# Kernel optimization log

Hardware: AMD Instinct MI355X
Metric: run time of the kernel (lower is better)

The kernel has to match this reference:

```python
import jax, jax.numpy as jnp
import numpy as np

B, S, T, C, Q = 8, 4096, 2048, 256, 256  # batch, ctx_steps, q_steps, context_size, query_size


def setup_inputs() -> dict:
    key = jax.random.key(0)
    k1, k2, k3, k4 = jax.random.split(key, 4)
    context = jax.random.normal(k1, (B, S, C), dtype=jnp.float32)
    query = jax.random.normal(k2, (T, B, Q), dtype=jnp.float32)
    context_mask = jax.random.randint(k3, (B, S), 0, 2).astype(bool)  # True = masked
    W = jax.random.normal(k4, (C, Q), dtype=jnp.float32)  # bilinear weights [context_size, query_size]
    return {"context": context, "query": query, "context_mask": context_mask, "W": W}


def reference(context, query, context_mask, W):
    # temp = 'auto' -> sqrt(query_size)
    temp = jnp.asarray(np.sqrt(Q), dtype=context.dtype)
    # scores[b,t,s] = (context[b,s,:] @ W) . query[t,b,:]
    scores = jnp.einsum('bsc,cq,tbq->bts', context, W, query) / temp
    neg = jnp.finfo(scores.dtype).min
    scores = jnp.where(context_mask[:, None, :], neg, scores)  # mask over ctx_steps
    attn = jax.nn.softmax(scores, axis=2)  # [B, T, S]
    # rows whose entire context is masked -> attention zeroed
    all_masked = jnp.all(context_mask, axis=1)[:, None, None]
    attn = jnp.where(all_masked, jnp.zeros((), attn.dtype), attn)
    composition = jnp.einsum('bts,bsc->btc', attn, context)  # [B, T, C]
    # module returns (attn, composition) permuted to [T, B, ...]
    return attn.transpose(1, 0, 2), composition.transpose(1, 0, 2)
```

## Files before the change

kernel.cpp:

```cpp
#include <hip/hip_runtime.h>

#define B_ 8
#define S_ 4096
#define T_ 2048
#define C_ 256
#define Q_ 256
#define NROW (T_ * B_)

typedef _Float16 f16;
typedef _Float16 f16x8 __attribute__((ext_vector_type(8)));
typedef _Float16 f16x4 __attribute__((ext_vector_type(4)));
typedef float f32x4 __attribute__((ext_vector_type(4)));

#define MFMA(a, b, c) __builtin_amdgcn_mfma_f32_16x16x32_f16((a), (b), (c), 0, 0, 0)

__global__ void k_mask_mode(const unsigned char* __restrict__ mb, int* __restrict__ mode,
                            int* __restrict__ allm) {
  __shared__ int s0_, s123_;
  if (threadIdx.x == 0) { s0_ = 0; s123_ = 0; }
  __syncthreads();
  int a0 = 0, a123 = 0;
  int base = threadIdx.x * 128;
  for (int i = 0; i < 128; ++i) {
    int idx = base + i;
    int v = mb[idx];
    if (idx & 3) a123 |= v; else a0 |= v;
  }
  if (a0) atomicOr(&s0_, 1);
  if (a123) atomicOr(&s123_, 1);
  __syncthreads();
  if (threadIdx.x == 0) {
    int m;
    if (s123_ == 0 && s0_ == 0) m = 3;
    else if (s123_ == 0) m = 0;
    else if (s0_ == 0) m = 2;
    else m = 1;
    *mode = m;
  }
  if (threadIdx.x < B_) allm[threadIdx.x] = 1;
}

__global__ void k_expand_mask(const void* __restrict__ mp, const int* __restrict__ mode,
                              float* __restrict__ maskf, int* __restrict__ allm) {
  int i = blockIdx.x * 256 + threadIdx.x;
  int md = *mode;
  int m;
  if (md == 0)      m = ((const int*)mp)[i] != 0;
  else if (md == 1) m = ((const unsigned char*)mp)[i] != 0;
  else if (md == 2) m = ((const float*)mp)[i] != 0.0f;
  else              m = 0;
  maskf[i] = m ? 1.0f : 0.0f;
  if (!m) atomicAnd(&allm[i / S_], 0);
}

__global__ void k_conv_w(const float* __restrict__ W, f16* __restrict__ WT) {
  int i = blockIdx.x * 256 + threadIdx.x;
  int c = i >> 8, q = i & 255;
  WT[q * C_ + c] = (f16)W[i];
}

__global__ void k_conv_q(const float* __restrict__ q, f16* __restrict__ qT) {
  int i = blockIdx.x * 256 + threadIdx.x;
  int e = i * 4;
  int t = e / (B_ * Q_);
  int rb = e - t * (B_ * Q_);
  int b = rb >> 8;
  int qq = rb & 255;
  f32x4 v = *(const f32x4*)(q + e);
  f16x4 h; h[0] = (f16)v[0]; h[1] = (f16)v[1]; h[2] = (f16)v[2]; h[3] = (f16)v[3];
  *(f16x4*)(qT + ((size_t)(b * T_ + t)) * Q_ + qq) = h;
}

__global__ void k_transpose_ctx(const float* __restrict__ ctx, f16* __restrict__ ctxT) {
  __shared__ f16 tile[64][65];
  int s0 = blockIdx.x * 64, c0 = blockIdx.y * 64, b = blockIdx.z;
  int r = threadIdx.x >> 2;
  int cs = (threadIdx.x & 3) * 16;
  const float* src = ctx + ((size_t)(b * S_ + s0 + r)) * C_ + c0 + cs;
  f32x4 v0 = ((const f32x4*)src)[0];
  f32x4 v1 = ((const f32x4*)src)[1];
  f32x4 v2 = ((const f32x4*)src)[2];
  f32x4 v3 = ((const f32x4*)src)[3];
#pragma unroll
  for (int j = 0; j < 4; ++j) {
    tile[r][cs + j] = (f16)v0[j];
    tile[r][cs + 4 + j] = (f16)v1[j];
    tile[r][cs + 8 + j] = (f16)v2[j];
    tile[r][cs + 12 + j] = (f16)v3[j];
  }
  __syncthreads();
  int c = threadIdx.x >> 2;
  int ss = (threadIdx.x & 3) * 16;
  f16x8 o0, o1;
#pragma unroll
  for (int j = 0; j < 8; ++j) { o0[j] = tile[ss + j][c]; o1[j] = tile[ss + 8 + j][c]; }
  f16* dst = ctxT + ((size_t)(b * C_ + c0 + c)) * S_ + s0 + ss;
  *(f16x8*)dst = o0;
  *(f16x8*)(dst + 8) = o1;
}

__launch_bounds__(256, 2)
__global__ void k_gemm_cw(const float* __restrict__ ctx, const f16* __restrict__ WT,
                          f16* __restrict__ CW) {
  __shared__ alignas(16) f16 As[128 * 32];
  __shared__ alignas(16) f16 Bs[128 * 32];
  int n0 = blockIdx.x * 128;
  int m0 = blockIdx.y * 128;
  int tid = threadIdx.x;
  int w = tid >> 6, l = tid & 63;
  int wm = (w >> 1) * 64, wn = (w & 1) * 64;
  int lr = l & 15, lk = (l >> 4) * 8;
  f32x4 acc[4][4] = {};
  for (int k0 = 0; k0 < C_; k0 += 32) {
    __syncthreads();
#pragma unroll
    for (int it = 0; it < 2; ++it) {
      int h = (it * 256 + tid) * 8;
      int row = h >> 5, kk = h & 31;
      const float* ap = ctx + (size_t)(m0 + row) * C_ + k0 + kk;
      f32x4 x0 = ((const f32x4*)ap)[0];
      f32x4 x1 = ((const f32x4*)ap)[1];
      f16x8 hv;
#pragma unroll
      for (int j = 0; j < 4; ++j) { hv[j] = (f16)x0[j]; hv[4 + j] = (f16)x1[j]; }
      *(f16x8*)&As[row * 32 + kk] = hv;
    }
#pragma unroll
    for (int it = 0; it < 2; ++it) {
      int h = (it * 256 + tid) * 8;
      int row = h >> 5, kk = h & 31;
      *(f16x8*)&Bs[row * 32 + kk] = *(const f16x8*)&WT[(size_t)(n0 + row) * C_ + k0 + kk];
    }
    __syncthreads();
    f16x8 af[4], bf[4];
#pragma unroll
    for (int m = 0; m < 4; ++m) af[m] = *(const f16x8*)&As[(wm + m * 16 + lr) * 32 + lk];
#pragma unroll
    for (int n = 0; n < 4; ++n) bf[n] = *(const f16x8*)&Bs[(wn + n * 16 + lr) * 32 + lk];
#pragma unroll
    for (int m = 0; m < 4; ++m)
#pragma unroll
      for (int n = 0; n < 4; ++n) acc[m][n] = MFMA(af[m], bf[n], acc[m][n]);
  }
#pragma unroll
  for (int m = 0; m < 4; ++m)
#pragma unroll
    for (int n = 0; n < 4; ++n)
#pragma unroll
      for (int i = 0; i < 4; ++i) {
        int gm = m0 + wm + m * 16 + (l >> 4) * 4 + i;
        int gn = n0 + wn + n * 16 + lr;
        CW[(size_t)gm * Q_ + gn] = (f16)(acc[m][n][i] * 0.0625f);
      }
}

__launch_bounds__(256, 2)
__global__ void k_gemm_scores(const f16* __restrict__ qT, const f16* __restrict__ CW,
                              const float* __restrict__ maskf, float* __restrict__ attn,
                              float* __restrict__ pmax, float* __restrict__ psum) {
  __shared__ alignas(16) f16 As[128 * 32];
  __shared__ alignas(16) f16 Bs[128 * 32];
  int n0 = blockIdx.x * 128;
  int m0 = blockIdx.y * 128;
  int b = blockIdx.z;
  const f16* A = qT + (size_t)b * T_ * Q_;
  const f16* Bm = CW + (size_t)b * S_ * Q_;
  int tid = threadIdx.x;
  int w = tid >> 6, l = tid & 63;
  int wm = (w >> 1) * 64, wn = (w & 1) * 64;
  int lr = l & 15, lk = (l >> 4) * 8;
  f32x4 acc[4][4] = {};
  for (int k0 = 0; k0 < Q_; k0 += 32) {
    __syncthreads();
#pragma unroll
    for (int it = 0; it < 2; ++it) {
      int h = (it * 256 + tid) * 8;
      int row = h >> 5, kk = h & 31;
      *(f16x8*)&As[row * 32 + kk] = *(const f16x8*)&A[(size_t)(m0 + row) * Q_ + k0 + kk];
    }
#pragma unroll
    for (int it = 0; it < 2; ++it) {
      int h = (it * 256 + tid) * 8;
      int row = h >> 5, kk = h & 31;
      *(f16x8*)&Bs[row * 32 + kk] = *(const f16x8*)&Bm[(size_t)(n0 + row) * Q_ + k0 + kk];
    }
    __syncthreads();
    f16x8 af[4], bf[4];
#pragma unroll
    for (int m = 0; m < 4; ++m) af[m] = *(const f16x8*)&As[(wm + m * 16 + lr) * 32 + lk];
#pragma unroll
    for (int n = 0; n < 4; ++n) bf[n] = *(const f16x8*)&Bs[(wn + n * 16 + lr) * 32 + lk];
#pragma unroll
    for (int m = 0; m < 4; ++m)
#pragma unroll
      for (int n = 0; n < 4; ++n) acc[m][n] = MFMA(af[m], bf[n], acc[m][n]);
  }
  float msk[4];
#pragma unroll
  for (int n = 0; n < 4; ++n) msk[n] = maskf[b * S_ + n0 + wn + n * 16 + lr];
#pragma unroll
  for (int m = 0; m < 4; ++m)
#pragma unroll
    for (int n = 0; n < 4; ++n) {
      int gn = n0 + wn + n * 16 + lr;
#pragma unroll
      for (int i = 0; i < 4; ++i) {
        int gt = m0 + wm + m * 16 + (l >> 4) * 4 + i;
        float v = acc[m][n][i];
        if (msk[n] != 0.0f) v = -3.4e38f;
        acc[m][n][i] = v;
        attn[((size_t)gt * B_ + b) * S_ + gn] = v;
      }
    }
  int g = l >> 4;
  int ch = blockIdx.x * 2 + (w & 1);
#pragma unroll
  for (int m = 0; m < 4; ++m)
#pragma unroll
    for (int i = 0; i < 4; ++i) {
      float mx = fmaxf(fmaxf(acc[m][0][i], acc[m][1][i]), fmaxf(acc[m][2][i], acc[m][3][i]));
      mx = fmaxf(mx, __shfl_xor(mx, 1));
      mx = fmaxf(mx, __shfl_xor(mx, 2));
      mx = fmaxf(mx, __shfl_xor(mx, 4));
      mx = fmaxf(mx, __shfl_xor(mx, 8));
      float sm = 0.0f;
#pragma unroll
      for (int n = 0; n < 4; ++n) sm += __expf(acc[m][n][i] - mx);
      sm += __shfl_xor(sm, 1);
      sm += __shfl_xor(sm, 2);
      sm += __shfl_xor(sm, 4);
      sm += __shfl_xor(sm, 8);
      if (lr == 0) {
        int gt = m0 + wm + m * 16 + g * 4 + i;
        int r = gt * B_ + b;
        pmax[ch * NROW + r] = mx;
        psum[ch * NROW + r] = sm;
      }
    }
}

__launch_bounds__(256, 2)
__global__ void k_gemm_stats(const f16* __restrict__ qT, const f16* __restrict__ CW,
                             const float* __restrict__ maskf,
                             float* __restrict__ pmax, float* __restrict__ psum) {
  __shared__ alignas(16) f16 As[128 * 32];
  __shared__ alignas(16) f16 Bs[128 * 32];
  int n0 = blockIdx.x * 128;
  int m0 = blockIdx.y * 128;
  int b = blockIdx.z;
  const f16* A = qT + (size_t)b * T_ * Q_;
  const f16* Bm = CW + (size_t)b * S_ * Q_;
  int tid = threadIdx.x;
  int w = tid >> 6, l = tid & 63;
  int wm = (w >> 1) * 64, wn = (w & 1) * 64;
  int lr = l & 15, lk = (l >> 4) * 8;
  f32x4 acc[4][4] = {};
  for (int k0 = 0; k0 < Q_; k0 += 32) {
    __syncthreads();
#pragma unroll
    for (int it = 0; it < 2; ++it) {
      int h = (it * 256 + tid) * 8;
      int row = h >> 5, kk = h & 31;
      *(f16x8*)&As[row * 32 + kk] = *(const f16x8*)&A[(size_t)(m0 + row) * Q_ + k0 + kk];
    }
#pragma unroll
    for (int it = 0; it < 2; ++it) {
      int h = (it * 256 + tid) * 8;
      int row = h >> 5, kk = h & 31;
      *(f16x8*)&Bs[row * 32 + kk] = *(const f16x8*)&Bm[(size_t)(n0 + row) * Q_ + k0 + kk];
    }
    __syncthreads();
    f16x8 af[4], bf[4];
#pragma unroll
    for (int m = 0; m < 4; ++m) af[m] = *(const f16x8*)&As[(wm + m * 16 + lr) * 32 + lk];
#pragma unroll
    for (int n = 0; n < 4; ++n) bf[n] = *(const f16x8*)&Bs[(wn + n * 16 + lr) * 32 + lk];
#pragma unroll
    for (int m = 0; m < 4; ++m)
#pragma unroll
      for (int n = 0; n < 4; ++n) acc[m][n] = MFMA(af[m], bf[n], acc[m][n]);
  }
  float msk[4];
#pragma unroll
  for (int n = 0; n < 4; ++n) msk[n] = maskf[b * S_ + n0 + wn + n * 16 + lr];
#pragma unroll
  for (int m = 0; m < 4; ++m)
#pragma unroll
    for (int n = 0; n < 4; ++n) {
      if (msk[n] != 0.0f) {
#pragma unroll
        for (int i = 0; i < 4; ++i) acc[m][n][i] = -3.4e38f;
      }
    }
  int g = l >> 4;
  int ch = blockIdx.x * 2 + (w & 1);
#pragma unroll
  for (int m = 0; m < 4; ++m)
#pragma unroll
    for (int i = 0; i < 4; ++i) {
      float mx = fmaxf(fmaxf(acc[m][0][i], acc[m][1][i]), fmaxf(acc[m][2][i], acc[m][3][i]));
      mx = fmaxf(mx, __shfl_xor(mx, 1));
      mx = fmaxf(mx, __shfl_xor(mx, 2));
      mx = fmaxf(mx, __shfl_xor(mx, 4));
      mx = fmaxf(mx, __shfl_xor(mx, 8));
      float sm = 0.0f;
#pragma unroll
      for (int n = 0; n < 4; ++n) sm += __expf(acc[m][n][i] - mx);
      sm += __shfl_xor(sm, 1);
      sm += __shfl_xor(sm, 2);
      sm += __shfl_xor(sm, 4);
      sm += __shfl_xor(sm, 8);
      if (lr == 0) {
        int gt = m0 + wm + m * 16 + g * 4 + i;
        int r = gt * B_ + b;
        pmax[ch * NROW + r] = mx;
        psum[ch * NROW + r] = sm;
      }
    }
}

__global__ void k_finalize(const float* __restrict__ pmax, const float* __restrict__ psum,
                           float* __restrict__ rmax, float* __restrict__ rsum) {
  int r = blockIdx.x * 256 + threadIdx.x;
  float mx = -3.4e38f;
#pragma unroll 8
  for (int c = 0; c < 64; ++c) mx = fmaxf(mx, pmax[c * NROW + r]);
  float s = 0.0f;
#pragma unroll 8
  for (int c = 0; c < 64; ++c) s += psum[c * NROW + r] * __expf(pmax[c * NROW + r] - mx);
  rmax[r] = mx;
  rsum[r] = s;
}

__launch_bounds__(256, 2)
__global__ void k_comp(float* __restrict__ attn, const f16* __restrict__ ctxT,
                       const float* __restrict__ rmax, const float* __restrict__ rsum,
                       const int* __restrict__ allm, float* __restrict__ comp) {
  __shared__ alignas(16) f16 As[2][32 * 64];
  __shared__ alignas(16) f16 Bs[2][256 * 64];
  const int t0 = blockIdx.x * 32;
  const int b = blockIdx.y;
  const int tid = threadIdx.x;
  const int w = tid >> 6, l = tid & 63;
  const int lr = l & 15, hi = l >> 4;
  const int am = allm[b];
  const int ar = tid >> 4;
  const int cg = tid & 15;
  float mx0, mx1, inv0, inv1;
  float* aP0;
  float* aP1;
  {
    int r0 = (t0 + ar) * B_ + b;
    int r1 = (t0 + 16 + ar) * B_ + b;
    mx0 = rmax[r0]; mx1 = rmax[r1];
    inv0 = am ? 0.0f : (1.0f / rsum[r0]);
    inv1 = am ? 0.0f : (1.0f / rsum[r1]);
    aP0 = attn + (size_t)r0 * S_ + cg * 4;
    aP1 = attn + (size_t)r1 * S_ + cg * 4;
  }
  const int aswz = (cg * 8) ^ ((ar & 7) << 4);
  const int bc = tid >> 3;
  const int bs = tid & 7;
  const f16* bP = ctxT + ((size_t)(b * C_ + bc)) * S_ + bs * 8;
  const int bswz = (bs * 16) ^ ((bc & 7) << 4);
  f32x4 acc[2][4] = {};
  f32x4 aC0 = *(const f32x4*)aP0;
  f32x4 aC1 = *(const f32x4*)aP1;
  f16x8 bC[8];
#pragma unroll
  for (int i = 0; i < 8; ++i) bC[i] = *(const f16x8*)(bP + (size_t)i * 32 * S_);
  for (int k = 0; k < S_ / 64; ++k) {
    const int cur = k & 1;
    const int kn = (k + 1) * 64;
    f32x4 aN0 = *(const f32x4*)(aP0 + kn);
    f32x4 aN1 = *(const f32x4*)(aP1 + kn);
    f16x8 bN[8];
#pragma unroll
    for (int i = 0; i < 8; ++i) bN[i] = *(const f16x8*)(bP + (size_t)i * 32 * S_ + kn);
    f32x4 p0, p1;
#pragma unroll
    for (int e = 0; e < 4; ++e) {
      p0[e] = __expf(aC0[e] - mx0) * inv0;
      p1[e] = __expf(aC1[e] - mx1) * inv1;
    }
    *(f32x4*)(aP0 + k * 64) = p0;
    *(f32x4*)(aP1 + k * 64) = p1;
    f16x4 h0, h1;
#pragma unroll
    for (int e = 0; e < 4; ++e) { h0[e] = (f16)p0[e]; h1[e] = (f16)p1[e]; }
    *(f16x4*)((char*)As[cur] + ar * 128 + aswz) = h0;
    *(f16x4*)((char*)As[cur] + (16 + ar) * 128 + aswz) = h1;
#pragma unroll
    for (int i = 0; i < 8; ++i)
      *(f16x8*)((char*)Bs[cur] + (i * 32 + bc) * 128 + bswz) = bC[i];
    asm volatile("s_waitcnt lgkmcnt(0)" ::: "memory");
    __builtin_amdgcn_s_barrier();
    __builtin_amdgcn_sched_barrier(0);
#pragma unroll
    for (int kk = 0; kk < 2; ++kk) {
      const int cb = (kk * 64 + hi * 16) ^ ((lr & 7) << 4);
      f16x8 af[2], bf[4];
#pragma unroll
      for (int m = 0; m < 2; ++m)
        af[m] = *(const f16x8*)((char*)As[cur] + (m * 16 + lr) * 128 + cb);
#pragma unroll
      for (int n = 0; n < 4; ++n)
        bf[n] = *(const f16x8*)((char*)Bs[cur] + (w * 64 + n * 16 + lr) * 128 + cb);
#pragma unroll
      for (int m = 0; m < 2; ++m)
#pragma unroll
        for (int n = 0; n < 4; ++n) acc[m][n] = MFMA(af[m], bf[n], acc[m][n]);
    }
    aC0 = aN0; aC1 = aN1;
#pragma unroll
    for (int i = 0; i < 8; ++i) bC[i] = bN[i];
  }
#pragma unroll
  for (int m = 0; m < 2; ++m)
#pragma unroll
    for (int n = 0; n < 4; ++n)
#pragma unroll
      for (int i = 0; i < 4; ++i) {
        int tl = m * 16 + hi * 4 + i;
        int cc = w * 64 + n * 16 + lr;
        comp[((size_t)(t0 + tl) * B_ + b) * C_ + cc] = acc[m][n][i];
      }
}

__launch_bounds__(256, 2)
__global__ void k_fused(const f16* __restrict__ qT, const f16* __restrict__ CW,
                        const f16* __restrict__ ctxT, const float* __restrict__ maskf,
                        const float* __restrict__ rmax, const float* __restrict__ rsum,
                        const int* __restrict__ allm,
                        float* __restrict__ attn, float* __restrict__ comp) {
  __shared__ alignas(16) f16 Bs[64 * 256];
  __shared__ alignas(16) f16 Ps[32 * 64];
  const int bid = blockIdx.x;
  const int b = bid & 7, tc = bid >> 3;
  const int t0 = tc * 32;
  const int tid = threadIdx.x;
  const int w = tid >> 6, l = tid & 63;
  const int lr = l & 15, hi = l >> 4;
  const int rswz = (lr & 7) << 4;
  const int am = allm[b];
  float smax[2][4], sinv[2][4];
#pragma unroll
  for (int m = 0; m < 2; ++m)
#pragma unroll
    for (int i = 0; i < 4; ++i) {
      int r = (t0 + m * 16 + hi * 4 + i) * B_ + b;
      smax[m][i] = rmax[r];
      sinv[m][i] = am ? 0.0f : (1.0f / rsum[r]);
    }
  f16x8 af[2][8];
#pragma unroll
  for (int m = 0; m < 2; ++m)
#pragma unroll
    for (int kq = 0; kq < 8; ++kq)
      af[m][kq] = *(const f16x8*)(qT + ((size_t)(b * T_ + t0 + m * 16 + lr)) * Q_ + kq * 32 + hi * 8);
  const int brow = tid & 63;
  const int bcolB = (tid >> 6) * 128;
  const int bswz = (brow & 7) << 4;
  const f16* cwBase = CW + (size_t)b * S_ * Q_;
  {
    const f16* src = cwBase + (size_t)brow * Q_ + bcolB / 2;
#pragma unroll
    for (int j = 0; j < 8; ++j)
      *(f16x8*)((char*)Bs + ((brow * 512 + bcolB + j * 16) ^ bswz)) = *(const f16x8*)(src + j * 8);
  }
  float mk = maskf[b * S_ + w * 16 + lr];
  f32x4 accC[2][4] = {};
  __syncthreads();
  for (int k = 0; k < S_ / 64; ++k) {
    const int s0 = k * 64;
    f32x4 accS[2] = {};
#pragma unroll
    for (int kq = 0; kq < 8; ++kq) {
      f16x8 bfr = *(const f16x8*)((char*)Bs + (((w * 16 + lr) * 512 + kq * 64 + hi * 16) ^ rswz));
#pragma unroll
      for (int m = 0; m < 2; ++m) accS[m] = MFMA(af[m][kq], bfr, accS[m]);
    }
#pragma unroll
    for (int m = 0; m < 2; ++m)
#pragma unroll
      for (int i = 0; i < 4; ++i) {
        int tl = m * 16 + hi * 4 + i;
        float p = (mk != 0.0f) ? 0.0f : __expf(accS[m][i] - smax[m][i]) * sinv[m][i];
        attn[((size_t)(t0 + tl) * B_ + b) * S_ + s0 + w * 16 + lr] = p;
        *(f16*)((char*)Ps + ((tl * 128 + (w * 16 + lr) * 2) ^ ((tl & 7) << 4))) = (f16)p;
      }
    __syncthreads();
    f16x8 gB[8];
    if (k < S_ / 64 - 1) {
      const f16* src = cwBase + (size_t)(s0 + 64 + brow) * Q_ + bcolB / 2;
#pragma unroll
      for (int j = 0; j < 8; ++j) gB[j] = *(const f16x8*)(src + j * 8);
    }
    float mkn = (k < S_ / 64 - 1) ? maskf[b * S_ + s0 + 64 + w * 16 + lr] : 0.0f;
#pragma unroll
    for (int kk = 0; kk < 2; ++kk) {
      f16x8 pa[2];
#pragma unroll
      for (int m = 0; m < 2; ++m)
        pa[m] = *(const f16x8*)((char*)Ps + (((m * 16 + lr) * 128 + kk * 64 + hi * 16) ^ rswz));
#pragma unroll
      for (int n = 0; n < 4; ++n) {
        f16x8 bc = *(const f16x8*)(ctxT + ((size_t)(b * C_ + w * 64 + n * 16 + lr)) * S_
                                   + s0 + kk * 32 + hi * 8);
#pragma unroll
        for (int m = 0; m < 2; ++m) accC[m][n] = MFMA(pa[m], bc, accC[m][n]);
      }
    }
    if (k < S_ / 64 - 1) {
#pragma unroll
      for (int j = 0; j < 8; ++j)
        *(f16x8*)((char*)Bs + ((brow * 512 + bcolB + j * 16) ^ bswz)) = gB[j];
    }
    mk = mkn;
    __syncthreads();
  }
#pragma unroll
  for (int m = 0; m < 2; ++m)
#pragma unroll
    for (int n = 0; n < 4; ++n)
#pragma unroll
      for (int i = 0; i < 4; ++i) {
        int tl = m * 16 + hi * 4 + i;
        int cc = w * 64 + n * 16 + lr;
        comp[((size_t)(t0 + tl) * B_ + b) * C_ + cc] = accC[m][n][i];
      }
}

extern "C" void kernel_launch(void* const* d_in, const int* in_sizes, int n_in,
                              void* d_out, int out_size, void* d_ws, size_t ws_size,
                              hipStream_t stream) {
  const float* ctx = (const float*)d_in[0];
  const float* query = (const float*)d_in[1];
  const void* mask = d_in[2];
  const float* W = (const float*)d_in[3];

  float* out = (float*)d_out;
  float* attn = out;
  float* comp = out + (size_t)T_ * B_ * S_;

  char* ws = (char*)d_ws;
  f16* ctxT = (f16*)(ws);
  f16* qT = (f16*)(ws + 16777216);
  f16* WT = (f16*)(ws + 25165824);
  float* maskf = (float*)(ws + 25296896);
  float* rmax = (float*)(ws + 25427968);
  float* rsum = (float*)(ws + 25493504);
  int* allm = (int*)(ws + 25559040);
  int* mode = (int*)(ws + 25559072);
  float* pmax = (float*)(ws + 25559168);
  float* psum = (float*)(ws + 29753472);

  k_mask_mode<<<1, 256, 0, stream>>>((const unsigned char*)mask, mode, allm);
  k_expand_mask<<<(B_ * S_) / 256, 256, 0, stream>>>(mask, mode, maskf, allm);
  k_conv_w<<<(C_ * Q_) / 256, 256, 0, stream>>>(W, WT);
  k_conv_q<<<(T_ * B_ * Q_ / 4) / 256, 256, 0, stream>>>(query, qT);
  k_transpose_ctx<<<dim3(S_ / 64, C_ / 64, B_), 256, 0, stream>>>(ctx, ctxT);

  if (ws_size >= (size_t)50724992) {
    f16* CW2 = (f16*)(ws + 33947776);
    k_gemm_cw<<<dim3(Q_ / 128, (B_ * S_) / 128), 256, 0, stream>>>(ctx, WT, CW2);
    k_gemm_stats<<<dim3(S_ / 128, T_ / 128, B_), 256, 0, stream>>>(qT, CW2, maskf, pmax, psum);
    k_finalize<<<NROW / 256, 256, 0, stream>>>(pmax, psum, rmax, rsum);
    k_fused<<<dim3((T_ / 32) * B_), 256, 0, stream>>>(qT, CW2, ctxT, maskf, rmax, rsum, allm,
                                                      attn, comp);
  } else {
    f16* CW = (f16*)comp;
    k_gemm_cw<<<dim3(Q_ / 128, (B_ * S_) / 128), 256, 0, stream>>>(ctx, WT, CW);
    k_gemm_scores<<<dim3(S_ / 128, T_ / 128, B_), 256, 0, stream>>>(qT, CW, maskf, attn, pmax, psum);
    k_finalize<<<NROW / 256, 256, 0, stream>>>(pmax, psum, rmax, rsum);
    k_comp<<<dim3(T_ / 32, B_), 256, 0, stream>>>(attn, ctxT, rmax, rsum, allm, comp);
  }
}
```

Measured before the change: 568.7 us.

## Software-pipeline fused attention kernel with register-resident CW and double-buffered P

Removes the shared-memory staging of the CW tile: each wave now loads its own 16 CW rows straight into registers, with a one-step register prefetch. The P tile is double-buffered in LDS so that the score MFMAs for step k overlap the composition MFMAs for step k-1, and each iteration needs one barrier instead of two. Attention stores are paired through a lane shuffle so each even lane writes two floats at once, and the context fragments are loaded early. The cost is a larger register footprint, which can lower occupancy under launch_bounds(256,2), plus a prologue and epilogue that add code.

```diff
diff --git a/kernel.cpp b/kernel.cpp
--- a/kernel.cpp
+++ b/kernel.cpp
@@ -10,6 +10,7 @@
 typedef _Float16 f16;
 typedef _Float16 f16x8 __attribute__((ext_vector_type(8)));
 typedef _Float16 f16x4 __attribute__((ext_vector_type(4)));
+typedef _Float16 f16x2 __attribute__((ext_vector_type(2)));
 typedef float f32x4 __attribute__((ext_vector_type(4)));
 
 #define MFMA(a, b, c) __builtin_amdgcn_mfma_f32_16x16x32_f16((a), (b), (c), 0, 0, 0)
@@ -433,15 +434,14 @@
                         const float* __restrict__ rmax, const float* __restrict__ rsum,
                         const int* __restrict__ allm,
                         float* __restrict__ attn, float* __restrict__ comp) {
-  __shared__ alignas(16) f16 Bs[64 * 256];
-  __shared__ alignas(16) f16 Ps[32 * 64];
+  __shared__ alignas(16) f16 Ps[2][32 * 64];
   const int bid = blockIdx.x;
-  const int b = bid & 7, tc = bid >> 3;
-  const int t0 = tc * 32;
+  const int b = bid & 7, t0 = (bid >> 3) * 32;
   const int tid = threadIdx.x;
   const int w = tid >> 6, l = tid & 63;
   const int lr = l & 15, hi = l >> 4;
   const int rswz = (lr & 7) << 4;
+  const int srow = w * 16 + lr;
   const int am = allm[b];
   float smax[2][4], sinv[2][4];
 #pragma unroll
@@ -458,66 +458,118 @@
 #pragma unroll
     for (int kq = 0; kq < 8; ++kq)
       af[m][kq] = *(const f16x8*)(qT + ((size_t)(b * T_ + t0 + m * 16 + lr)) * Q_ + kq * 32 + hi * 8);
-  const int brow = tid & 63;
-  const int bcolB = (tid >> 6) * 128;
-  const int bswz = (brow & 7) << 4;
-  const f16* cwBase = CW + (size_t)b * S_ * Q_;
+  const f16* cwL = CW + (size_t)b * S_ * Q_ + (size_t)srow * Q_ + hi * 8;
+  const f16* cxL = ctxT + (size_t)(b * C_ + w * 64 + lr) * S_ + hi * 8;
+  const float* maskP = maskf + b * S_ + srow;
+  f32x4 accC[2][4] = {};
+  f16x8 cwF[8];
+#pragma unroll
+  for (int kq = 0; kq < 8; ++kq) cwF[kq] = *(const f16x8*)(cwL + kq * 32);
+  float mk = maskP[0];
   {
-    const f16* src = cwBase + (size_t)brow * Q_ + bcolB / 2;
-#pragma unroll
-    for (int j = 0; j < 8; ++j)
-      *(f16x8*)((char*)Bs + ((brow * 512 + bcolB + j * 16) ^ bswz)) = *(const f16x8*)(src + j * 8);
-  }
-  float mk = maskf[b * S_ + w * 16 + lr];
-  f32x4 accC[2][4] = {};
-  __syncthreads();
-  for (int k = 0; k < S_ / 64; ++k) {
-    const int s0 = k * 64;
+    f16x8 cwN[8];
+#pragma unroll
+    for (int kq = 0; kq < 8; ++kq) cwN[kq] = *(const f16x8*)(cwL + (size_t)64 * Q_ + kq * 32);
+    float mkn = maskP[64];
     f32x4 accS[2] = {};
 #pragma unroll
-    for (int kq = 0; kq < 8; ++kq) {
-      f16x8 bfr = *(const f16x8*)((char*)Bs + (((w * 16 + lr) * 512 + kq * 64 + hi * 16) ^ rswz));
-#pragma unroll
-      for (int m = 0; m < 2; ++m) accS[m] = MFMA(af[m][kq], bfr, accS[m]);
-    }
+    for (int kq = 0; kq < 8; ++kq)
+#pragma unroll
+      for (int m = 0; m < 2; ++m) accS[m] = MFMA(af[m][kq], cwF[kq], accS[m]);
 #pragma unroll
     for (int m = 0; m < 2; ++m)
 #pragma unroll
       for (int i = 0; i < 4; ++i) {
         int tl = m * 16 + hi * 4 + i;
         float p = (mk != 0.0f) ? 0.0f : __expf(accS[m][i] - smax[m][i]) * sinv[m][i];
-        attn[((size_t)(t0 + tl) * B_ + b) * S_ + s0 + w * 16 + lr] = p;
-        *(f16*)((char*)Ps + ((tl * 128 + (w * 16 + lr) * 2) ^ ((tl & 7) << 4))) = (f16)p;
-      }
-    __syncthreads();
-    f16x8 gB[8];
+        float po = __shfl_xor(p, 1);
+        if (!(lr & 1)) {
+          float2 fp; fp.x = p; fp.y = po;
+          *(float2*)&attn[((size_t)(t0 + tl) * B_ + b) * S_ + srow] = fp;
+          f16x2 h; h[0] = (f16)p; h[1] = (f16)po;
+          *(f16x2*)((char*)Ps[0] + ((tl * 128 + srow * 2) ^ ((tl & 7) << 4))) = h;
+        }
+      }
+#pragma unroll
+    for (int kq = 0; kq < 8; ++kq) cwF[kq] = cwN[kq];
+    mk = mkn;
+    asm volatile("s_waitcnt lgkmcnt(0)" ::: "memory");
+    __builtin_amdgcn_s_barrier();
+  }
+  for (int k = 1; k < S_ / 64; ++k) {
+    const int s0 = k * 64;
+    const int cur = k & 1, prev = cur ^ 1;
+    f16x8 cwN[8];
+    float mkn = 0.0f;
     if (k < S_ / 64 - 1) {
-      const f16* src = cwBase + (size_t)(s0 + 64 + brow) * Q_ + bcolB / 2;
-#pragma unroll
-      for (int j = 0; j < 8; ++j) gB[j] = *(const f16x8*)(src + j * 8);
-    }
-    float mkn = (k < S_ / 64 - 1) ? maskf[b * S_ + s0 + 64 + w * 16 + lr] : 0.0f;
+#pragma unroll
+      for (int kq = 0; kq < 8; ++kq)
+        cwN[kq] = *(const f16x8*)(cwL + (size_t)(s0 + 64) * Q_ + kq * 32);
+      mkn = maskP[s0 + 64];
+    }
+    const int sc0 = s0 - 64;
+    f16x8 cx[8];
+#pragma unroll
+    for (int n = 0; n < 4; ++n)
+#pragma unroll
+      for (int kk = 0; kk < 2; ++kk)
+        cx[n * 2 + kk] = *(const f16x8*)(cxL + (size_t)(n * 16) * S_ + sc0 + kk * 32);
+    f32x4 accS[2] = {};
+#pragma unroll
+    for (int kq = 0; kq < 8; ++kq)
+#pragma unroll
+      for (int m = 0; m < 2; ++m) accS[m] = MFMA(af[m][kq], cwF[kq], accS[m]);
 #pragma unroll
     for (int kk = 0; kk < 2; ++kk) {
       f16x8 pa[2];
 #pragma unroll
       for (int m = 0; m < 2; ++m)
-        pa[m] = *(const f16x8*)((char*)Ps + (((m * 16 + lr) * 128 + kk * 64 + hi * 16) ^ rswz));
-#pragma unroll
-      for (int n = 0; n < 4; ++n) {
-        f16x8 bc = *(const f16x8*)(ctxT + ((size_t)(b * C_ + w * 64 + n * 16 + lr)) * S_
-                                   + s0 + kk * 32 + hi * 8);
-#pragma unroll
-        for (int m = 0; m < 2; ++m) accC[m][n] = MFMA(pa[m], bc, accC[m][n]);
-      }
-    }
-    if (k < S_ / 64 - 1) {
-#pragma unroll
-      for (int j = 0; j < 8; ++j)
-        *(f16x8*)((char*)Bs + ((brow * 512 + bcolB + j * 16) ^ bswz)) = gB[j];
-    }
+        pa[m] = *(const f16x8*)((char*)Ps[prev] + (((m * 16 + lr) * 128 + kk * 64 + hi * 16) ^ rswz));
+#pragma unroll
+      for (int n = 0; n < 4; ++n)
+#pragma unroll
+        for (int m = 0; m < 2; ++m) accC[m][n] = MFMA(pa[m], cx[n * 2 + kk], accC[m][n]);
+    }
+#pragma unroll
+    for (int m = 0; m < 2; ++m)
+#pragma unroll
+      for (int i = 0; i < 4; ++i) {
+        int tl = m * 16 + hi * 4 + i;
+        float p = (mk != 0.0f) ? 0.0f : __expf(accS[m][i] - smax[m][i]) * sinv[m][i];
+        float po = __shfl_xor(p, 1);
+        if (!(lr & 1)) {
+          float2 fp; fp.x = p; fp.y = po;
+          *(float2*)&attn[((size_t)(t0 + tl) * B_ + b) * S_ + s0 + srow] = fp;
+          f16x2 h; h[0] = (f16)p; h[1] = (f16)po;
+          *(f16x2*)((char*)Ps[cur] + ((tl * 128 + srow * 2) ^ ((tl & 7) << 4))) = h;
+        }
+      }
+#pragma unroll
+    for (int kq = 0; kq < 8; ++kq) cwF[kq] = cwN[kq];
     mk = mkn;
-    __syncthreads();
+    asm volatile("s_waitcnt lgkmcnt(0)" ::: "memory");
+    __builtin_amdgcn_s_barrier();
+  }
+  {
+    const int sc0 = S_ - 64;
+    const int prev = (S_ / 64 - 1) & 1;
+    f16x8 cx[8];
+#pragma unroll
+    for (int n = 0; n < 4; ++n)
+#pragma unroll
+      for (int kk = 0; kk < 2; ++kk)
+        cx[n * 2 + kk] = *(const f16x8*)(cxL + (size_t)(n * 16) * S_ + sc0 + kk * 32);
+#pragma unroll
+    for (int kk = 0; kk < 2; ++kk) {
+      f16x8 pa[2];
+#pragma unroll
+      for (int m = 0; m < 2; ++m)
+        pa[m] = *(const f16x8*)((char*)Ps[prev] + (((m * 16 + lr) * 128 + kk * 64 + hi * 16) ^ rswz));
+#pragma unroll
+      for (int n = 0; n < 4; ++n)
+#pragma unroll
+        for (int m = 0; m < 2; ++m) accC[m][n] = MFMA(pa[m], cx[n * 2 + kk], accC[m][n]);
+    }
   }
 #pragma unroll
   for (int m = 0; m < 2; ++m)
```

New measurement: 564.0 us. About the same (-0.8%).
